# Optimization experiments

Hardware: AMD Instinct MI355X
Metric: run time of the kernel (lower is better)

The kernel has to match this reference:

```python
import jax, jax.numpy as jnp
import numpy as np

B, N, T, F = 8, 2000, 64, 32
H = 128    # lstm_hidden
GH = 128   # gnn_hidden
E = 32000  # edges


def setup_inputs() -> dict:
    key = jax.random.key(0)
    ks = jax.random.split(key, 12)
    s = 0.05
    return {
        "x": jax.random.normal(ks[0], (B, N, T, F), jnp.float32),
        "edge_index": jax.random.randint(ks[1], (2, E), 0, N, dtype=jnp.int32),
        # LSTM params (torch gate order i, f, g, o)
        "Wih": jax.random.normal(ks[2], (4 * H, F), jnp.float32) * s,
        "Whh": jax.random.normal(ks[3], (4 * H, H), jnp.float32) * s,
        "bih": jax.random.normal(ks[4], (4 * H,), jnp.float32) * s,
        "bhh": jax.random.normal(ks[5], (4 * H,), jnp.float32) * s,
        # GCNConv params
        "gcn_W": jax.random.normal(ks[6], (H, GH), jnp.float32) * s,
        "gcn_b": jax.random.normal(ks[7], (GH,), jnp.float32) * s,
        # shared MLP head
        "mlp_W1": jax.random.normal(ks[8], (GH, GH // 2), jnp.float32) * s,
        "mlp_b1": jax.random.normal(ks[9], (GH // 2,), jnp.float32) * s,
        "mlp_W2": jax.random.normal(ks[10], (GH // 2, 1), jnp.float32) * s,
        "mlp_b2": jax.random.normal(ks[11], (1,), jnp.float32) * s,
    }


def _lstm_last_h(x, Wih, Whh, bih, bhh):
    # x: [M, T, F] -> last hidden state [M, H]
    M = x.shape[0]
    xg = jnp.einsum('mtf,gf->mtg', x, Wih) + bih  # precompute input gates [M, T, 4H]

    def step(carry, xg_t):
        h, c = carry
        z = xg_t + h @ Whh.T + bhh
        i, f, g, o = jnp.split(z, 4, axis=-1)
        i = jax.nn.sigmoid(i)
        f = jax.nn.sigmoid(f)
        g = jnp.tanh(g)
        o = jax.nn.sigmoid(o)
        c = f * c + i * g
        h = o * jnp.tanh(c)
        return (h, c), None

    h0 = jnp.zeros((M, H), x.dtype)
    c0 = jnp.zeros((M, H), x.dtype)
    (h, _), _ = jax.lax.scan(step, (h0, c0), jnp.swapaxes(xg, 0, 1))
    return h


def reference(x, edge_index, Wih, Whh, bih, bhh, gcn_W, gcn_b,
              mlp_W1, mlp_b1, mlp_W2, mlp_b2):
    Bx, Nx, Tx, Fx = x.shape
    # LSTM over all B*N node sequences, take last hidden state
    h = _lstm_last_h(x.reshape(Bx * Nx, Tx, Fx), Wih, Whh, bih, bhh)
    node_features = h.reshape(Bx, Nx, H)

    # GCNConv (PyG semantics): add self-loops, symmetric normalization
    loops = jnp.arange(Nx, dtype=edge_index.dtype)
    src = jnp.concatenate([edge_index[0], loops])
    dst = jnp.concatenate([edge_index[1], loops])
    deg = jnp.zeros((Nx,), x.dtype).at[dst].add(1.0)
    dinv = jnp.where(deg > 0, jax.lax.rsqrt(deg), 0.0)
    norm = dinv[src] * dinv[dst]  # [E+N]

    xw = node_features @ gcn_W                     # [B, N, GH]
    msgs = xw[:, src, :] * norm[None, :, None]     # gather + scale [B, E+N, GH]
    agg = jnp.zeros((Bx, Nx, GH), x.dtype).at[:, dst, :].add(msgs) + gcn_b

    # shared MLP head (dropout is identity in eval mode)
    h1 = jax.nn.silu(agg @ mlp_W1 + mlp_b1)
    out = h1 @ mlp_W2 + mlp_b2                     # [B, N, 1]
    return out.squeeze(-1)                         # [B, N]
```

## Files before the change

kernel.cpp:

```cpp
#include <hip/hip_runtime.h>

typedef _Float16 f16x8 __attribute__((ext_vector_type(8)));
typedef _Float16 f16x4 __attribute__((ext_vector_type(4)));
typedef _Float16 f16x2 __attribute__((ext_vector_type(2)));
typedef float f32x4 __attribute__((ext_vector_type(4)));

#define NB_   8
#define NN_   2000
#define TT_   64
#define FF_   32
#define HH_   128
#define EE_   32000
#define KD    160
#define RSTR  192
#define NODES 32
#define WXSTR 40

__device__ __forceinline__ float fexp2(float v) { return __builtin_amdgcn_exp2f(v); }
__device__ __forceinline__ float frcp(float v)  { return __builtin_amdgcn_rcpf(v); }

__global__ void prep_kernel(const float* __restrict__ Wih, const float* __restrict__ Whh,
                            const float* __restrict__ bih, const float* __restrict__ bhh,
                            const float* __restrict__ gcnW,
                            _Float16* __restrict__ W16, _Float16* __restrict__ Wg16,
                            float* __restrict__ bias, float* __restrict__ deg) {
  int idx = blockIdx.x * 256 + threadIdx.x;
  if (idx < 512 * KD) {
    int col = idx / KD, k = idx % KD;
    float v = (k < 32) ? Wih[col * 32 + k] : Whh[col * 128 + (k - 32)];
    float sc = (col >= 256 && col < 384) ? -2.88539008f : -1.44269504f;
    W16[idx] = (_Float16)(v * sc);
  } else if (idx < 512 * KD + 128 * 128) {
    int i2 = idx - 512 * KD;
    int colg = i2 >> 7, k = i2 & 127;
    Wg16[i2] = (_Float16)gcnW[k * 128 + colg];
  } else if (idx < 512 * KD + 128 * 128 + 512) {
    int i3 = idx - (512 * KD + 128 * 128);
    float sc = (i3 >= 256 && i3 < 384) ? -2.88539008f : -1.44269504f;
    bias[i3] = (bih[i3] + bhh[i3]) * sc;
  } else if (idx < 512 * KD + 128 * 128 + 512 + NN_) {
    deg[idx - (512 * KD + 128 * 128 + 512)] = 0.f;
  }
}

__global__ void deg_kernel(const int* __restrict__ ei, float* __restrict__ deg) {
  int e = blockIdx.x * 256 + threadIdx.x;
  if (e < EE_ + NN_) {
    int d = (e < EE_) ? ei[EE_ + e] : (e - EE_);
    atomicAdd(&deg[d], 1.f);
  }
}

__global__ void scan_kernel(const float* __restrict__ deg, int* __restrict__ offs,
                            int* __restrict__ cursor, float* __restrict__ dinv) {
  __shared__ int s0[2048], s1[2048];
  int t = threadIdx.x;
  for (int i = t; i < 2048; i += 1024) s0[i] = (i < NN_) ? ((int)deg[i] - 1) : 0;
  __syncthreads();
  int* src = s0; int* dst = s1;
  for (int off = 1; off < 2048; off <<= 1) {
    for (int i = t; i < 2048; i += 1024)
      dst[i] = src[i] + ((i >= off) ? src[i - off] : 0);
    __syncthreads();
    int* tmp = src; src = dst; dst = tmp;
  }
  for (int i = t; i < NN_; i += 1024) {
    int exc = src[i] - ((int)deg[i] - 1);
    offs[i] = exc;
    cursor[i] = exc;
    float d = deg[i];
    dinv[i] = (d > 0.f) ? __builtin_amdgcn_rsqf(d) : 0.f;
  }
}

__global__ void fill_kernel(const int* __restrict__ ei, const float* __restrict__ dinv,
                            int* __restrict__ cursor, int* __restrict__ csr_src,
                            float* __restrict__ csr_w) {
  int e = blockIdx.x * 256 + threadIdx.x;
  if (e >= EE_) return;
  int s = ei[e], d = ei[EE_ + e];
  int pos = atomicAdd(&cursor[d], 1);
  csr_src[pos] = s;
  csr_w[pos] = dinv[s] * dinv[d];
}

__global__ __launch_bounds__(512, 4) void lstm_gcn_kernel(
    const float* __restrict__ x, const _Float16* __restrict__ W16,
    const float* __restrict__ bias, const _Float16* __restrict__ Wg16,
    float* __restrict__ xwT) {
  __shared__ _Float16 A[NODES * RSTR];
  __shared__ _Float16 WxL[512 * WXSTR];
  __shared__ float    BiasL[512];
  const int tid  = threadIdx.x;
  const int wave = tid >> 6;
  const int lane = tid & 63;
  const int n15  = lane & 15;
  const int q    = lane >> 4;
  const int m    = n15 & 7;
  const int hm   = m >> 2;
  const int qx   = q ^ (m & 3);
  const int node0 = blockIdx.x * NODES;

  f16x8 Af[4][4];
#pragma unroll
  for (int g = 0; g < 4; ++g) {
    const int row = g * 128 + wave * 16 + n15;
#pragma unroll
    for (int kc = 1; kc < 5; ++kc)
      Af[g][kc - 1] = *(const f16x8*)(W16 + row * KD + kc * 32 + q * 8);
  }
  {
    const _Float16* wr = W16 + tid * KD;
#pragma unroll
    for (int cch = 0; cch < 4; ++cch)
      *(f16x8*)(WxL + tid * WXSTR + cch * 8) = *(const f16x8*)(wr + cch * 8);
    if (tid < 128) *(float4*)(BiasL + tid * 4) = *(const float4*)(bias + tid * 4);
  }

  const int bRow = n15 * RSTR + (qx << 3);
  const int hOff = n15 * RSTR + (((4 + 2 * wave + (q >> 1)) ^ m) << 3) + ((q & 1) << 2);
  const int aRow = (wave * 16 + n15) * WXSTR + q * 8;

  const int xrow = tid >> 4;
  const int xf   = (tid & 15) * 2;
  const int xOff = xrow * RSTR + (((xf >> 3) ^ (xrow & 7)) << 3) + (xf & 7);
  const float* xb = x + (size_t)(node0 + xrow) * (TT_ * FF_) + xf;

  {
    int row = tid >> 4, ci = tid & 15;
    f16x8 z8 = {(_Float16)0, (_Float16)0, (_Float16)0, (_Float16)0,
                (_Float16)0, (_Float16)0, (_Float16)0, (_Float16)0};
    *(f16x8*)(A + row * RSTR + (((4 + ci) ^ (row & 7)) << 3)) = z8;
  }
  {
    float2 v = *(const float2*)xb;
    f16x2 p = {(_Float16)v.x, (_Float16)v.y};
    *(f16x2*)(A + xOff) = p;
  }
  __syncthreads();

  if ((blockIdx.x ^ (blockIdx.x >> 8)) & 1) __builtin_amdgcn_s_sleep(40);

  f32x4 acc[2][4], c[2];
  c[0] = (f32x4){0, 0, 0, 0};
  c[1] = (f32x4){0, 0, 0, 0};

  for (int t = 0; t < TT_; ++t) {
    {
#pragma unroll
      for (int nt = 0; nt < 2; ++nt)
#pragma unroll
        for (int g = 0; g < 4; ++g)
          acc[nt][g] = *(const f32x4*)(BiasL + g * 128 + wave * 16 + q * 4);
      f16x8 ax[4];
#pragma unroll
      for (int g = 0; g < 4; ++g)
        ax[g] = *(const f16x8*)(WxL + g * 128 * WXSTR + aRow);
      __builtin_amdgcn_s_setprio(1);
#pragma unroll
      for (int nt = 0; nt < 2; ++nt) {
        f16x8 bf = *(const f16x8*)(A + nt * (16 * RSTR) + bRow + (hm << 5));
#pragma unroll
        for (int g = 0; g < 4; ++g)
          acc[nt][g] = __builtin_amdgcn_mfma_f32_16x16x32_f16(ax[g], bf, acc[nt][g], 0, 0, 0);
      }
#pragma unroll
      for (int kc = 1; kc < 5; ++kc)
#pragma unroll
        for (int nt = 0; nt < 2; ++nt) {
          f16x8 bf = *(const f16x8*)(A + nt * (16 * RSTR) + bRow + ((kc ^ hm) << 5));
#pragma unroll
          for (int g = 0; g < 4; ++g)
            acc[nt][g] = __builtin_amdgcn_mfma_f32_16x16x32_f16(Af[g][kc - 1], bf, acc[nt][g], 0, 0, 0);
        }
      __builtin_amdgcn_s_setprio(0);
    }
    const bool more = (t + 1 < TT_);
    float2 xv;
    if (more) xv = *(const float2*)(xb + (t + 1) * FF_);
    __syncthreads();

#pragma unroll
    for (int nt = 0; nt < 2; ++nt) {
      f16x4 hp;
#pragma unroll
      for (int r = 0; r < 4; ++r) {
        float Ei = fexp2(acc[nt][0][r]);
        float Ef = fexp2(acc[nt][1][r]);
        float Eg = fexp2(acc[nt][2][r]);
        float Eo = fexp2(acc[nt][3][r]);
        float ai = 1.f + Ei, af = 1.f + Ef, ag = 1.f + Eg, ao = 1.f + Eo;
        float pig = ai * ag;
        float num = c[nt][r] * pig + (1.f - Eg) * af;
        float cn  = num * frcp(af * pig);
        c[nt][r] = cn;
        float Ec = fexp2(-2.88539008f * cn);
        float hn = (1.f - Ec) * frcp((1.f + Ec) * ao);
        hp[r] = (_Float16)hn;
      }
      *(f16x4*)(A + nt * (16 * RSTR) + hOff) = hp;
    }
    if (more) { f16x2 p = {(_Float16)xv.x, (_Float16)xv.y}; *(f16x2*)(A + xOff) = p; }
    __syncthreads();
  }

  f16x8 Ag[4];
#pragma unroll
  for (int kc = 0; kc < 4; ++kc)
    Ag[kc] = *(const f16x8*)(Wg16 + (wave * 16 + n15) * HH_ + kc * 32 + q * 8);
  f32x4 acc2[2];
  acc2[0] = (f32x4){0, 0, 0, 0};
  acc2[1] = (f32x4){0, 0, 0, 0};
  __builtin_amdgcn_s_setprio(1);
#pragma unroll
  for (int kc = 0; kc < 4; ++kc)
#pragma unroll
    for (int nt = 0; nt < 2; ++nt) {
      f16x8 bf = *(const f16x8*)(A + nt * (16 * RSTR) + bRow + (((kc + 1) ^ hm) << 5));
      acc2[nt] = __builtin_amdgcn_mfma_f32_16x16x32_f16(Ag[kc], bf, acc2[nt], 0, 0, 0);
    }
  __builtin_amdgcn_s_setprio(0);
#pragma unroll
  for (int nt = 0; nt < 2; ++nt) {
    int mnode = node0 + nt * 16 + n15;
    int b = mnode / NN_;
    int n = mnode - b * NN_;
    *(float4*)(xwT + ((size_t)n * 8 + b) * HH_ + wave * 16 + q * 4) =
        (float4){acc2[nt][0], acc2[nt][1], acc2[nt][2], acc2[nt][3]};
  }
}

__global__ __launch_bounds__(256) void gathermlp_kernel(
    const float* __restrict__ xwT, const int* __restrict__ offs,
    const float* __restrict__ deg, const float* __restrict__ dinv,
    const int* __restrict__ csr_src, const float* __restrict__ csr_w,
    const float* __restrict__ gcnb,
    const float* __restrict__ W1, const float* __restrict__ b1,
    const float* __restrict__ W2, const float* __restrict__ b2,
    float* __restrict__ out) {
  __shared__ float aggs[8][128];
  __shared__ float W1T[64][132];
  const int d = blockIdx.x;
  const int tid = threadIdx.x;
  for (int i = tid; i < 8192; i += 256) {
    int k = i >> 6, j = i & 63;
    W1T[j][k] = W1[i];
  }
  {
    const int j  = tid & 127;
    const int bh = tid >> 7;
    const int beg = offs[d];
    const int cnt = (int)deg[d] - 1;
    const int boff = bh * 512 + j;
    float a0 = 0.f, a1 = 0.f, a2 = 0.f, a3 = 0.f;
    int e = 0;
    for (; e + 1 < cnt; e += 2) {
      int s0 = csr_src[beg + e],     s1 = csr_src[beg + e + 1];
      float w0 = csr_w[beg + e],     w1 = csr_w[beg + e + 1];
      const float* p0 = xwT + (size_t)s0 * 1024 + boff;
      const float* p1 = xwT + (size_t)s1 * 1024 + boff;
      float v00 = p0[0], v01 = p0[128], v02 = p0[256], v03 = p0[384];
      float v10 = p1[0], v11 = p1[128], v12 = p1[256], v13 = p1[384];
      a0 += w0 * v00 + w1 * v10;
      a1 += w0 * v01 + w1 * v11;
      a2 += w0 * v02 + w1 * v12;
      a3 += w0 * v03 + w1 * v13;
    }
    if (e < cnt) {
      int s = csr_src[beg + e];
      float w = csr_w[beg + e];
      const float* p = xwT + (size_t)s * 1024 + boff;
      a0 += w * p[0]; a1 += w * p[128]; a2 += w * p[256]; a3 += w * p[384];
    }
    {
      float di = dinv[d];
      float w = di * di;
      const float* p = xwT + (size_t)d * 1024 + boff;
      a0 += w * p[0]; a1 += w * p[128]; a2 += w * p[256]; a3 += w * p[384];
    }
    float bj = gcnb[j];
    aggs[bh * 4 + 0][j] = a0 + bj;
    aggs[bh * 4 + 1][j] = a1 + bj;
    aggs[bh * 4 + 2][j] = a2 + bj;
    aggs[bh * 4 + 3][j] = a3 + bj;
  }
  __syncthreads();
  const int b = tid >> 5;
  const int t = tid & 31;
  float acc1 = b1[t], acc2 = b1[t + 32];
#pragma unroll 8
  for (int kc = 0; kc < 32; ++kc) {
    float4 a  = *(const float4*)&aggs[b][kc * 4];
    float4 w1 = *(const float4*)&W1T[t][kc * 4];
    float4 w2 = *(const float4*)&W1T[t + 32][kc * 4];
    acc1 += a.x * w1.x + a.y * w1.y + a.z * w1.z + a.w * w1.w;
    acc2 += a.x * w2.x + a.y * w2.y + a.z * w2.z + a.w * w2.w;
  }
  float s1 = acc1 * frcp(1.f + fexp2(-1.44269504f * acc1));
  float s2 = acc2 * frcp(1.f + fexp2(-1.44269504f * acc2));
  float part = s1 * W2[t] + s2 * W2[t + 32];
#pragma unroll
  for (int msk = 16; msk >= 1; msk >>= 1) part += __shfl_xor(part, msk);
  if (t == 0) out[(size_t)b * NN_ + d] = part + b2[0];
}

extern "C" void kernel_launch(void* const* d_in, const int* in_sizes, int n_in,
                              void* d_out, int out_size, void* d_ws, size_t ws_size,
                              hipStream_t stream) {
  const float* x    = (const float*)d_in[0];
  const int*   ei   = (const int*)d_in[1];
  const float* Wih  = (const float*)d_in[2];
  const float* Whh  = (const float*)d_in[3];
  const float* bih  = (const float*)d_in[4];
  const float* bhh  = (const float*)d_in[5];
  const float* gcnW = (const float*)d_in[6];
  const float* gcnb = (const float*)d_in[7];
  const float* W1   = (const float*)d_in[8];
  const float* b1   = (const float*)d_in[9];
  const float* W2   = (const float*)d_in[10];
  const float* b2   = (const float*)d_in[11];
  float* out = (float*)d_out;
  char* ws = (char*)d_ws;

  _Float16* W16    = (_Float16*)(ws);
  _Float16* Wg16   = (_Float16*)(ws + 163840);
  float*    bias   = (float*)(ws + 196608);
  float*    xwT    = (float*)(ws + 198656);
  float*    deg    = (float*)(ws + 8390656);
  float*    dinv   = (float*)(ws + 8398848);
  int*      offs   = (int*)(ws + 8407040);
  int*      cursor = (int*)(ws + 8415232);
  int*      csrs   = (int*)(ws + 8423424);
  float*    csrw   = (float*)(ws + 8551424);

  prep_kernel<<<394, 256, 0, stream>>>(Wih, Whh, bih, bhh, gcnW, W16, Wg16, bias, deg);
  deg_kernel<<<133, 256, 0, stream>>>(ei, deg);
  scan_kernel<<<1, 1024, 0, stream>>>(deg, offs, cursor, dinv);
  fill_kernel<<<125, 256, 0, stream>>>(ei, dinv, cursor, csrs, csrw);
  lstm_gcn_kernel<<<500, 512, 0, stream>>>(x, W16, bias, Wg16, xwT);
  gathermlp_kernel<<<NN_, 256, 0, stream>>>(xwT, offs, deg, dinv, csrs, csrw,
                                            gcnb, W1, b1, W2, b2, out);
}
```

Baseline: 399.3 us.

## Fuse degree histogram into scan kernel, vectorize gather loads, hoist x prefetch

The degree counting moves into the single-block scan kernel as a shared-memory histogram, which removes the deg zeroing and the separate global-atomic deg kernel launch. The gather in gathermlp now has each thread load a float4 of contiguous columns and unrolls over four neighbours, so memory accesses are wider and there is more memory-level parallelism. In the LSTM loop, the next-timestep x load is issued before the MFMA block rather than after it, which gives that load more time to hide its latency. The histogram now runs on one workgroup over 32K edges, which could cost more than the parallel atomic version it replaces.

```diff
diff --git a/kernel.cpp b/kernel.cpp
--- a/kernel.cpp
+++ b/kernel.cpp
@@ -23,7 +23,7 @@
                             const float* __restrict__ bih, const float* __restrict__ bhh,
                             const float* __restrict__ gcnW,
                             _Float16* __restrict__ W16, _Float16* __restrict__ Wg16,
-                            float* __restrict__ bias, float* __restrict__ deg) {
+                            float* __restrict__ bias) {
   int idx = blockIdx.x * 256 + threadIdx.x;
   if (idx < 512 * KD) {
     int col = idx / KD, k = idx % KD;
@@ -38,24 +38,20 @@
     int i3 = idx - (512 * KD + 128 * 128);
     float sc = (i3 >= 256 && i3 < 384) ? -2.88539008f : -1.44269504f;
     bias[i3] = (bih[i3] + bhh[i3]) * sc;
-  } else if (idx < 512 * KD + 128 * 128 + 512 + NN_) {
-    deg[idx - (512 * KD + 128 * 128 + 512)] = 0.f;
-  }
-}
-
-__global__ void deg_kernel(const int* __restrict__ ei, float* __restrict__ deg) {
-  int e = blockIdx.x * 256 + threadIdx.x;
-  if (e < EE_ + NN_) {
-    int d = (e < EE_) ? ei[EE_ + e] : (e - EE_);
-    atomicAdd(&deg[d], 1.f);
-  }
-}
-
-__global__ void scan_kernel(const float* __restrict__ deg, int* __restrict__ offs,
-                            int* __restrict__ cursor, float* __restrict__ dinv) {
+  }
+}
+
+__global__ void scan_kernel(const int* __restrict__ ei, int* __restrict__ offs,
+                            int* __restrict__ cursor, float* __restrict__ dinv,
+                            float* __restrict__ deg) {
+  __shared__ int hist[2048];
   __shared__ int s0[2048], s1[2048];
   int t = threadIdx.x;
-  for (int i = t; i < 2048; i += 1024) s0[i] = (i < NN_) ? ((int)deg[i] - 1) : 0;
+  for (int i = t; i < 2048; i += 1024) hist[i] = (i < NN_) ? 1 : 0;
+  __syncthreads();
+  for (int e = t; e < EE_; e += 1024) atomicAdd(&hist[ei[EE_ + e]], 1);
+  __syncthreads();
+  for (int i = t; i < 2048; i += 1024) s0[i] = (i < NN_) ? (hist[i] - 1) : 0;
   __syncthreads();
   int* src = s0; int* dst = s1;
   for (int off = 1; off < 2048; off <<= 1) {
@@ -65,11 +61,13 @@
     int* tmp = src; src = dst; dst = tmp;
   }
   for (int i = t; i < NN_; i += 1024) {
-    int exc = src[i] - ((int)deg[i] - 1);
+    int dgi = hist[i];
+    int exc = src[i] - (dgi - 1);
     offs[i] = exc;
     cursor[i] = exc;
-    float d = deg[i];
-    dinv[i] = (d > 0.f) ? __builtin_amdgcn_rsqf(d) : 0.f;
+    float dg = (float)dgi;
+    deg[i] = dg;
+    dinv[i] = __builtin_amdgcn_rsqf(dg);
   }
 }
 
@@ -146,12 +144,19 @@
   c[1] = (f32x4){0, 0, 0, 0};
 
   for (int t = 0; t < TT_; ++t) {
+    const bool more = (t + 1 < TT_);
+    float2 xv;
+    if (more) xv = *(const float2*)(xb + (t + 1) * FF_);
+
     {
+      f32x4 bt[4];
+#pragma unroll
+      for (int g = 0; g < 4; ++g)
+        bt[g] = *(const f32x4*)(BiasL + g * 128 + wave * 16 + q * 4);
 #pragma unroll
       for (int nt = 0; nt < 2; ++nt)
 #pragma unroll
-        for (int g = 0; g < 4; ++g)
-          acc[nt][g] = *(const f32x4*)(BiasL + g * 128 + wave * 16 + q * 4);
+        for (int g = 0; g < 4; ++g) acc[nt][g] = bt[g];
       f16x8 ax[4];
 #pragma unroll
       for (int g = 0; g < 4; ++g)
@@ -175,9 +180,6 @@
         }
       __builtin_amdgcn_s_setprio(0);
     }
-    const bool more = (t + 1 < TT_);
-    float2 xv;
-    if (more) xv = *(const float2*)(xb + (t + 1) * FF_);
     __syncthreads();
 
 #pragma unroll
@@ -247,42 +249,41 @@
     W1T[j][k] = W1[i];
   }
   {
-    const int j  = tid & 127;
-    const int bh = tid >> 7;
     const int beg = offs[d];
     const int cnt = (int)deg[d] - 1;
-    const int boff = bh * 512 + j;
+    const int col = tid * 4;
     float a0 = 0.f, a1 = 0.f, a2 = 0.f, a3 = 0.f;
     int e = 0;
-    for (; e + 1 < cnt; e += 2) {
+    for (; e + 3 < cnt; e += 4) {
       int s0 = csr_src[beg + e],     s1 = csr_src[beg + e + 1];
+      int s2 = csr_src[beg + e + 2], s3 = csr_src[beg + e + 3];
       float w0 = csr_w[beg + e],     w1 = csr_w[beg + e + 1];
-      const float* p0 = xwT + (size_t)s0 * 1024 + boff;
-      const float* p1 = xwT + (size_t)s1 * 1024 + boff;
-      float v00 = p0[0], v01 = p0[128], v02 = p0[256], v03 = p0[384];
-      float v10 = p1[0], v11 = p1[128], v12 = p1[256], v13 = p1[384];
-      a0 += w0 * v00 + w1 * v10;
-      a1 += w0 * v01 + w1 * v11;
-      a2 += w0 * v02 + w1 * v12;
-      a3 += w0 * v03 + w1 * v13;
-    }
-    if (e < cnt) {
+      float w2 = csr_w[beg + e + 2], w3 = csr_w[beg + e + 3];
+      float4 v0 = *(const float4*)(xwT + (size_t)s0 * 1024 + col);
+      float4 v1 = *(const float4*)(xwT + (size_t)s1 * 1024 + col);
+      float4 v2 = *(const float4*)(xwT + (size_t)s2 * 1024 + col);
+      float4 v3 = *(const float4*)(xwT + (size_t)s3 * 1024 + col);
+      a0 += w0 * v0.x + w1 * v1.x + w2 * v2.x + w3 * v3.x;
+      a1 += w0 * v0.y + w1 * v1.y + w2 * v2.y + w3 * v3.y;
+      a2 += w0 * v0.z + w1 * v1.z + w2 * v2.z + w3 * v3.z;
+      a3 += w0 * v0.w + w1 * v1.w + w2 * v2.w + w3 * v3.w;
+    }
+    for (; e < cnt; ++e) {
       int s = csr_src[beg + e];
       float w = csr_w[beg + e];
-      const float* p = xwT + (size_t)s * 1024 + boff;
-      a0 += w * p[0]; a1 += w * p[128]; a2 += w * p[256]; a3 += w * p[384];
+      float4 v = *(const float4*)(xwT + (size_t)s * 1024 + col);
+      a0 += w * v.x; a1 += w * v.y; a2 += w * v.z; a3 += w * v.w;
     }
     {
       float di = dinv[d];
       float w = di * di;
-      const float* p = xwT + (size_t)d * 1024 + boff;
-      a0 += w * p[0]; a1 += w * p[128]; a2 += w * p[256]; a3 += w * p[384];
-    }
-    float bj = gcnb[j];
-    aggs[bh * 4 + 0][j] = a0 + bj;
-    aggs[bh * 4 + 1][j] = a1 + bj;
-    aggs[bh * 4 + 2][j] = a2 + bj;
-    aggs[bh * 4 + 3][j] = a3 + bj;
+      float4 v = *(const float4*)(xwT + (size_t)d * 1024 + col);
+      a0 += w * v.x; a1 += w * v.y; a2 += w * v.z; a3 += w * v.w;
+    }
+    const int jc = (tid & 31) * 4;
+    float4 bj = *(const float4*)(gcnb + jc);
+    float4 res = {a0 + bj.x, a1 + bj.y, a2 + bj.z, a3 + bj.w};
+    *(float4*)&aggs[tid >> 5][jc] = res;
   }
   __syncthreads();
   const int b = tid >> 5;
@@ -333,9 +334,8 @@
   int*      csrs   = (int*)(ws + 8423424);
   float*    csrw   = (float*)(ws + 8551424);
 
-  prep_kernel<<<394, 256, 0, stream>>>(Wih, Whh, bih, bhh, gcnW, W16, Wg16, bias, deg);
-  deg_kernel<<<133, 256, 0, stream>>>(ei, deg);
-  scan_kernel<<<1, 1024, 0, stream>>>(deg, offs, cursor, dinv);
+  prep_kernel<<<386, 256, 0, stream>>>(Wih, Whh, bih, bhh, gcnW, W16, Wg16, bias);
+  scan_kernel<<<1, 1024, 0, stream>>>(ei, offs, cursor, dinv, deg);
   fill_kernel<<<125, 256, 0, stream>>>(ei, dinv, cursor, csrs, csrw);
   lstm_gcn_kernel<<<500, 512, 0, stream>>>(x, W16, bias, Wg16, xwT);
   gathermlp_kernel<<<NN_, 256, 0, stream>>>(xwT, offs, deg, dinv, csrs, csrw,
```

After: 420.8 us. 5.4% more time.
